# Kernel tuning notes

Hardware: AMD Instinct MI355X
Metric: run time of the kernel (lower is better)

Reference implementation:

```python
import jax, jax.numpy as jnp
import numpy as np

B, S, E, H = 2, 2048, 1024, 16
D = E // H  # head_dim = 64
SCALE = 1.0 / np.sqrt(D)


def setup_inputs() -> dict:
    key = jax.random.key(0)
    ks = jax.random.split(key, 5)
    std = 0.02
    return {
        "x": jax.random.normal(ks[0], (B, S, E), dtype=jnp.float32),
        "wq": jax.random.normal(ks[1], (E, E), dtype=jnp.float32) * std,
        "wk": jax.random.normal(ks[2], (E, E), dtype=jnp.float32) * std,
        "wv": jax.random.normal(ks[3], (E, E), dtype=jnp.float32) * std,
        "wo": jax.random.normal(ks[4], (E, E), dtype=jnp.float32) * std,
    }


def reference(x, wq, wk, wv, wo):
    # Linear projections (torch Linear: y = x @ W.T); weights stored as [out, in]
    q = jnp.einsum('bse,fe->bsf', x, wq)
    k = jnp.einsum('bse,fe->bsf', x, wk)
    v = jnp.einsum('bse,fe->bsf', x, wv)
    # split heads -> [B, H, S, D]
    q = q.reshape(B, S, H, D).transpose(0, 2, 1, 3)
    k = k.reshape(B, S, H, D).transpose(0, 2, 1, 3)
    v = v.reshape(B, S, H, D).transpose(0, 2, 1, 3)
    # scaled dot-product scores [B, H, S, S]
    scores = jnp.einsum('bhqd,bhkd->bhqk', q, k) * SCALE
    # causal mask: -inf above diagonal
    causal = jnp.triu(jnp.full((S, S), -jnp.inf, dtype=scores.dtype), k=1)
    scores = scores + causal[None, None, :, :]
    attn = jax.nn.softmax(scores, axis=-1)
    # dropout p=0 -> identity
    out = jnp.einsum('bhqk,bhkd->bhqd', attn, v)
    out = out.transpose(0, 2, 1, 3).reshape(B, S, E)
    return jnp.einsum('bse,fe->bsf', out, wo)
```

## Files before the change

kernel.cpp:

```cpp
#include <hip/hip_runtime.h>
#include <hip/hip_bf16.h>

#define B_ 2
#define S_ 2048
#define E_ 1024
#define H_ 16
#define D_ 64
#define QKV_N 3072
#define C2_ 0.18033688011112042f

typedef __attribute__((ext_vector_type(8))) unsigned short ushort8_t;
typedef __attribute__((ext_vector_type(8))) short short8_t;
typedef __attribute__((ext_vector_type(4))) float f32x4;

__device__ __forceinline__ unsigned short f2b(float f) {
    union { float f; unsigned u; } x; x.f = f;
    unsigned r = x.u + 0x7FFFu + ((x.u >> 16) & 1u);
    return (unsigned short)(r >> 16);
}
__device__ __forceinline__ ushort2 pkbf(float a, float b) {
    union { __hip_bfloat162 h; ushort2 u; } c;
    c.h = __float22bfloat162_rn(make_float2(a, b));
    return c.u;
}
__device__ __forceinline__ void glds16(const unsigned short* g, unsigned short* l) {
    __builtin_amdgcn_global_load_lds((const __attribute__((address_space(1))) void*)g,
                                     (__attribute__((address_space(3))) void*)l, 16, 0, 0);
}

__global__ __launch_bounds__(256) void cast_all(const float* __restrict__ x,
                                                const float* __restrict__ wq,
                                                const float* __restrict__ wk,
                                                const float* __restrict__ wv,
                                                const float* __restrict__ wo,
                                                unsigned short* __restrict__ xb,
                                                unsigned short* __restrict__ wb) {
    int idx = blockIdx.x * 256 + threadIdx.x;
    const float* src; unsigned short* dst; float s = 1.f; int j;
    if (idx < 1048576) {
        src = x; dst = xb; j = idx;
    } else {
        j = idx - 1048576;
        int y = j >> 18;
        src = (y == 0) ? wq : (y == 1) ? wk : (y == 2) ? wv : wo;
        dst = wb + (size_t)y * 1048576;
        j &= 262143;
        if (y == 0) s = C2_;
    }
    float4 v = ((const float4*)src)[j];
    ushort2 lo = pkbf(v.x * s, v.y * s), hi = pkbf(v.z * s, v.w * s);
    ((ushort4*)dst)[j] = make_ushort4(lo.x, lo.y, hi.x, hi.y);
}

template <int TM, bool OUT_BF16, bool VT>
__device__ __forceinline__ void gemm_bt_body(const unsigned short* __restrict__ A,
                                             const unsigned short* __restrict__ Bt,
                                             void* __restrict__ Cout,
                                             int m0, int n0, int N, int K) {
    __shared__ unsigned short As[2 * TM * 32];
    __shared__ unsigned short Bs[2 * 128 * 32];
    const int tid = threadIdx.x;
    const int wave = tid >> 6;
    const int lane = tid & 63;
    const int wm = (wave >> 1) * (TM / 2);
    const int wn = (wave & 1) * 64;
    const int quad = lane >> 4;
    const int l15 = lane & 15;
    constexpr int MI = TM / 32;

    f32x4 acc[MI][4] = {};

    const int srow = lane >> 2;
    const int scb  = (lane & 3) * 8;
    const unsigned short* gB0 = Bt + (size_t)(n0 + wave * 32 + srow) * K + scb;
    const unsigned short* gB1 = gB0 + (size_t)16 * K;
    unsigned short* lB0 = Bs + wave * 1024;
    unsigned short* lB1 = lB0 + 512;
    const unsigned short* gA0;
    const unsigned short* gA1 = nullptr;
    unsigned short* lA0;
    unsigned short* lA1 = nullptr;
    if (TM == 128) {
        gA0 = A + (size_t)(m0 + wave * 32 + srow) * K + scb;
        gA1 = gA0 + (size_t)16 * K;
        lA0 = As + wave * 1024; lA1 = lA0 + 512;
    } else {
        gA0 = A + (size_t)(m0 + wave * 16 + srow) * K + scb;
        lA0 = As + wave * 512;
    }

    for (int k0 = 0; k0 < K; k0 += 64) {
        __syncthreads();
        glds16(gA0 + k0, lA0);
        glds16(gA0 + k0 + 32, lA0 + TM * 32);
        if (TM == 128) {
            glds16(gA1 + k0, lA1);
            glds16(gA1 + k0 + 32, lA1 + TM * 32);
        }
        glds16(gB0 + k0, lB0);
        glds16(gB0 + k0 + 32, lB0 + 128 * 32);
        glds16(gB1 + k0, lB1);
        glds16(gB1 + k0 + 32, lB1 + 128 * 32);
        __syncthreads();

#pragma unroll
        for (int h = 0; h < 2; ++h) {
            const unsigned short* ah = As + h * TM * 32;
            const unsigned short* bh = Bs + h * 128 * 32;
            short8_t af[MI], bfv[4];
#pragma unroll
            for (int mi = 0; mi < MI; ++mi)
                af[mi] = *(const short8_t*)(&ah[(wm + mi * 16 + l15) * 32 + quad * 8]);
#pragma unroll
            for (int ni = 0; ni < 4; ++ni)
                bfv[ni] = *(const short8_t*)(&bh[(wn + ni * 16 + l15) * 32 + quad * 8]);
#pragma unroll
            for (int mi = 0; mi < MI; ++mi)
#pragma unroll
                for (int ni = 0; ni < 4; ++ni)
                    acc[mi][ni] = __builtin_amdgcn_mfma_f32_16x16x32_bf16(
                        af[mi], bfv[ni], acc[mi][ni], 0, 0, 0);
        }
    }

    if (VT && n0 >= 2048) {
#pragma unroll
        for (int mi = 0; mi < MI; ++mi)
#pragma unroll
            for (int ni = 0; ni < 4; ++ni) {
                int col = n0 + wn + ni * 16 + l15;
                int r0  = m0 + wm + mi * 16 + quad * 4;
                int bb  = r0 >> 11, s = r0 & 2047;
                size_t drow = (size_t)bb * 2048 + 2 * (col - 2048) + (s >> 10);
                unsigned short* dp = (unsigned short*)Cout + drow * QKV_N + 2048 + (s & 1023);
                *(ushort4*)dp = make_ushort4(f2b(acc[mi][ni][0]), f2b(acc[mi][ni][1]),
                                             f2b(acc[mi][ni][2]), f2b(acc[mi][ni][3]));
            }
        return;
    }

#pragma unroll
    for (int mi = 0; mi < MI; ++mi)
#pragma unroll
        for (int ni = 0; ni < 4; ++ni)
#pragma unroll
            for (int r = 0; r < 4; ++r) {
                int row = m0 + wm + mi * 16 + quad * 4 + r;
                int col = n0 + wn + ni * 16 + l15;
                float val = acc[mi][ni][r];
                if (OUT_BF16)
                    ((unsigned short*)Cout)[(size_t)row * N + col] = f2b(val);
                else
                    ((float*)Cout)[(size_t)row * N + col] = val;
            }
}

__global__ __launch_bounds__(256, 3) void gemm_qkv(const unsigned short* __restrict__ xb,
                                                   const unsigned short* __restrict__ wqkv,
                                                   unsigned short* __restrict__ qkv) {
    int id = blockIdx.x + 24 * blockIdx.y;
    int sw = (id & 7) * 96 + (id >> 3);
    int n0 = (sw % 24) * 128;
    int m0 = (sw / 24) * 128;
    gemm_bt_body<128, true, true>(xb, wqkv, qkv, m0, n0, QKV_N, E_);
}

__global__ __launch_bounds__(256, 2) void gemm_out(const unsigned short* __restrict__ a,
                                                   const unsigned short* __restrict__ wob,
                                                   float* __restrict__ c) {
    gemm_bt_body<64, false, false>(a, wob, c, blockIdx.y * 64, blockIdx.x * 128, E_, E_);
}

__global__ __launch_bounds__(512, 4) void attn_kernel(const unsigned short* __restrict__ QKV,
                                                      unsigned short* __restrict__ O) {
    __shared__ unsigned short Ks[2][64 * 64];
    __shared__ unsigned short Vs[2][64 * 64];
    __shared__ unsigned short Ps[8][16 * 64];

    const int b = blockIdx.z, h = blockIdx.y;
    const int cx = blockIdx.x;
    const int c0 = (cx & 1) ? (15 - (cx >> 1)) : (cx >> 1);
    const int c = (b == 0) ? c0 : (15 - c0);
    const int tid = threadIdx.x;
    const int w = tid >> 6, lane = tid & 63;
    const int quad = lane >> 4, l15 = lane & 15;
    const int lx = l15 & 7;
    const int chunk = (w < 4) ? (31 - c) : c;
    const int Q0 = chunk * 64 + (w & 3) * 16;

    const size_t qo = (size_t)(b * S_ + Q0 + l15) * QKV_N + h * D_;
    short8_t bq0 = *(const short8_t*)(QKV + qo + quad * 8);
    short8_t bq1 = *(const short8_t*)(QKV + qo + 32 + quad * 8);

    f32x4 Oacc[4] = {};
    f32x4 Lacc = {};
    const int qg = Q0 + l15;
    short8_t ones;
#pragma unroll
    for (int i = 0; i < 8; ++i) ones[i] = (short)0x3F80;

    const int fo0 = ((quad) ^ lx) * 8;
    const int fo1 = ((4 + quad) ^ lx) * 8;
    const int krow = l15 * 64;
    int pwo[4];
#pragma unroll
    for (int tm = 0; tm < 4; ++tm)
        pwo[tm] = ((tm * 2 + (quad >> 1)) ^ lx) * 8 + (quad & 1) * 4;

    const int srow = tid >> 3;
    const int scb  = tid & 7;
    const int scw  = (scb ^ (srow & 7)) * 8;
    const int wofs = w * 512;
    const unsigned short* KsrcB = QKV + (size_t)(b * S_ + srow) * QKV_N + 1024 + h * D_ + scw;
    const unsigned short* VsrcB = QKV + (size_t)(b * S_ + 2 * (h * D_ + srow)) * QKV_N + 2048 + scw;

    auto issue = [&](int pn, int ktn) {
        glds16(KsrcB + (size_t)ktn * QKV_N, &Ks[pn][wofs]);
        glds16(VsrcB + (size_t)(ktn >> 10) * QKV_N + (ktn & 1023), &Vs[pn][wofs]);
    };

    const int ntiles = 32 - c;
    issue(0, 0);

    for (int t = 0; t < ntiles; ++t) {
        const int p = t & 1;
        const int kt = t * 64;
        __syncthreads();
        if (t + 1 < ntiles) issue(p ^ 1, kt + 64);
        __builtin_amdgcn_sched_barrier(0);

        if (kt > Q0 + 15) continue;
        const bool h2 = (kt + 32 <= Q0 + 15);

        if (kt + 63 <= Q0) {
#pragma unroll
            for (int tm = 0; tm < 4; ++tm) {
                short8_t ak0 = *(const short8_t*)(&Ks[p][tm * 1024 + krow + fo0]);
                short8_t ak1 = *(const short8_t*)(&Ks[p][tm * 1024 + krow + fo1]);
                f32x4 st = {0.f, 0.f, 0.f, 0.f};
                __builtin_amdgcn_s_setprio(1);
                st = __builtin_amdgcn_mfma_f32_16x16x32_bf16(ak0, bq0, st, 0, 0, 0);
                st = __builtin_amdgcn_mfma_f32_16x16x32_bf16(ak1, bq1, st, 0, 0, 0);
                __builtin_amdgcn_s_setprio(0);
                float p0 = __builtin_amdgcn_exp2f(st[0]);
                float p1 = __builtin_amdgcn_exp2f(st[1]);
                float p2 = __builtin_amdgcn_exp2f(st[2]);
                float p3 = __builtin_amdgcn_exp2f(st[3]);
                ushort2 a = pkbf(p0, p1), c2 = pkbf(p2, p3);
                *(ushort4*)(&Ps[w][krow + pwo[tm]]) = make_ushort4(a.x, a.y, c2.x, c2.y);
            }
        } else {
            const int need = h2 ? 4 : 2;
            for (int tm = 0; tm < need; ++tm) {
                if (kt + tm * 16 <= Q0 + 15) {
                    short8_t ak0 = *(const short8_t*)(&Ks[p][tm * 1024 + krow + fo0]);
                    short8_t ak1 = *(const short8_t*)(&Ks[p][tm * 1024 + krow + fo1]);
                    f32x4 st = {0.f, 0.f, 0.f, 0.f};
                    __builtin_amdgcn_s_setprio(1);
                    st = __builtin_amdgcn_mfma_f32_16x16x32_bf16(ak0, bq0, st, 0, 0, 0);
                    st = __builtin_amdgcn_mfma_f32_16x16x32_bf16(ak1, bq1, st, 0, 0, 0);
                    __builtin_amdgcn_s_setprio(0);
                    const int kvb = kt + tm * 16 + quad * 4;
                    float p0 = (kvb     > qg) ? 0.f : __builtin_amdgcn_exp2f(st[0]);
                    float p1 = (kvb + 1 > qg) ? 0.f : __builtin_amdgcn_exp2f(st[1]);
                    float p2 = (kvb + 2 > qg) ? 0.f : __builtin_amdgcn_exp2f(st[2]);
                    float p3 = (kvb + 3 > qg) ? 0.f : __builtin_amdgcn_exp2f(st[3]);
                    ushort2 a = pkbf(p0, p1), c2 = pkbf(p2, p3);
                    *(ushort4*)(&Ps[w][krow + pwo[tm]]) = make_ushort4(a.x, a.y, c2.x, c2.y);
                } else {
                    *(ushort4*)(&Ps[w][krow + pwo[tm]]) = make_ushort4(0, 0, 0, 0);
                }
            }
        }

#pragma unroll
        for (int kh = 0; kh < 2; ++kh) {
            if (kh == 1 && !h2) break;
            const int fo = kh ? fo1 : fo0;
            short8_t bv[4];
#pragma unroll
            for (int tn = 0; tn < 4; ++tn)
                bv[tn] = *(const short8_t*)(&Vs[p][tn * 1024 + krow + fo]);
            short8_t ap = *(const short8_t*)(&Ps[w][krow + fo]);
            __builtin_amdgcn_s_setprio(1);
#pragma unroll
            for (int tn = 0; tn < 4; ++tn)
                Oacc[tn] = __builtin_amdgcn_mfma_f32_16x16x32_bf16(
                    ap, bv[tn], Oacc[tn], 0, 0, 0);
            Lacc = __builtin_amdgcn_mfma_f32_16x16x32_bf16(ap, ones, Lacc, 0, 0, 0);
            __builtin_amdgcn_s_setprio(0);
        }
    }

    float lir[4];
#pragma unroll
    for (int r = 0; r < 4; ++r)
        lir[r] = 1.f / Lacc[r];
#pragma unroll
    for (int tn = 0; tn < 4; ++tn)
#pragma unroll
        for (int r = 0; r < 4; ++r) {
            int row = Q0 + quad * 4 + r;
            O[(size_t)(b * S_ + row) * E_ + h * D_ + tn * 16 + l15] =
                f2b(Oacc[tn][r] * lir[r]);
        }
}

extern "C" void kernel_launch(void* const* d_in, const int* in_sizes, int n_in,
                              void* d_out, int out_size, void* d_ws, size_t ws_size,
                              hipStream_t stream) {
    const float* x  = (const float*)d_in[0];
    const float* wq = (const float*)d_in[1];
    const float* wk = (const float*)d_in[2];
    const float* wv = (const float*)d_in[3];
    const float* wo = (const float*)d_in[4];
    float* out = (float*)d_out;

    unsigned short* ws   = (unsigned short*)d_ws;
    unsigned short* xb   = ws;
    unsigned short* wqkv = ws + 4194304;
    unsigned short* wob  = ws + 7340032;
    unsigned short* qkvb = ws + 8388608;
    unsigned short* ab   = ws + 20971520;

    cast_all<<<8192, 256, 0, stream>>>(x, wq, wk, wv, wo, xb, wqkv);
    gemm_qkv<<<dim3(24, 32), 256, 0, stream>>>(xb, wqkv, qkvb);
    attn_kernel<<<dim3(16, 16, 2), 512, 0, stream>>>(qkvb, ab);
    gemm_out<<<dim3(8, 64), 256, 0, stream>>>(ab, wob, out);
}
```

Measured before the change: 171.2 us.

## Triple-buffer K/V tiles in attention with vmcnt waits; swizzle out-projection block order

The attention kernel moves from double to triple buffering of K/V tiles in shared memory, prefetching two tiles ahead. The full __syncthreads is replaced by an explicit s_waitcnt vmcnt plus s_barrier, so loads for later tiles can stay in flight while the current tile is computed. The out-projection GEMM also gets a block-index swizzle to improve L2 reuse. The extra LDS buffers raise shared memory per block, which may cut occupancy. The hand-written vmcnt counts must match the number of outstanding global-to-LDS loads for correctness.

Result: faster. 167.0 us (-2.4%).

```diff
diff --git a/kernel.cpp b/kernel.cpp
--- a/kernel.cpp
+++ b/kernel.cpp
@@ -168,13 +168,15 @@
 __global__ __launch_bounds__(256, 2) void gemm_out(const unsigned short* __restrict__ a,
                                                    const unsigned short* __restrict__ wob,
                                                    float* __restrict__ c) {
-    gemm_bt_body<64, false, false>(a, wob, c, blockIdx.y * 64, blockIdx.x * 128, E_, E_);
+    int id = blockIdx.x + 8 * blockIdx.y;
+    int sw = (id & 7) * 64 + (id >> 3);
+    gemm_bt_body<64, false, false>(a, wob, c, (sw >> 3) * 64, (sw & 7) * 128, E_, E_);
 }
 
 __global__ __launch_bounds__(512, 4) void attn_kernel(const unsigned short* __restrict__ QKV,
                                                       unsigned short* __restrict__ O) {
-    __shared__ unsigned short Ks[2][64 * 64];
-    __shared__ unsigned short Vs[2][64 * 64];
+    __shared__ unsigned short Ks[3][64 * 64];
+    __shared__ unsigned short Vs[3][64 * 64];
     __shared__ unsigned short Ps[8][16 * 64];
 
     const int b = blockIdx.z, h = blockIdx.y;
@@ -214,82 +216,91 @@
     const unsigned short* KsrcB = QKV + (size_t)(b * S_ + srow) * QKV_N + 1024 + h * D_ + scw;
     const unsigned short* VsrcB = QKV + (size_t)(b * S_ + 2 * (h * D_ + srow)) * QKV_N + 2048 + scw;
 
-    auto issue = [&](int pn, int ktn) {
-        glds16(KsrcB + (size_t)ktn * QKV_N, &Ks[pn][wofs]);
-        glds16(VsrcB + (size_t)(ktn >> 10) * QKV_N + (ktn & 1023), &Vs[pn][wofs]);
+    auto issue = [&](int bn, int ktn) {
+        glds16(KsrcB + (size_t)ktn * QKV_N, &Ks[bn][wofs]);
+        glds16(VsrcB + (size_t)(ktn >> 10) * QKV_N + (ktn & 1023), &Vs[bn][wofs]);
     };
 
     const int ntiles = 32 - c;
     issue(0, 0);
+    issue(1, 64);
+    int bi = 0;
 
     for (int t = 0; t < ntiles; ++t) {
-        const int p = t & 1;
         const int kt = t * 64;
-        __syncthreads();
-        if (t + 1 < ntiles) issue(p ^ 1, kt + 64);
+        if (t + 1 < ntiles) asm volatile("s_waitcnt vmcnt(2)" ::: "memory");
+        else                asm volatile("s_waitcnt vmcnt(0)" ::: "memory");
+        __builtin_amdgcn_s_barrier();
         __builtin_amdgcn_sched_barrier(0);
-
-        if (kt > Q0 + 15) continue;
-        const bool h2 = (kt + 32 <= Q0 + 15);
-
-        if (kt + 63 <= Q0) {
-#pragma unroll
-            for (int tm = 0; tm < 4; ++tm) {
-                short8_t ak0 = *(const short8_t*)(&Ks[p][tm * 1024 + krow + fo0]);
-                short8_t ak1 = *(const short8_t*)(&Ks[p][tm * 1024 + krow + fo1]);
-                f32x4 st = {0.f, 0.f, 0.f, 0.f};
-                __builtin_amdgcn_s_setprio(1);
-                st = __builtin_amdgcn_mfma_f32_16x16x32_bf16(ak0, bq0, st, 0, 0, 0);
-                st = __builtin_amdgcn_mfma_f32_16x16x32_bf16(ak1, bq1, st, 0, 0, 0);
-                __builtin_amdgcn_s_setprio(0);
-                float p0 = __builtin_amdgcn_exp2f(st[0]);
-                float p1 = __builtin_amdgcn_exp2f(st[1]);
-                float p2 = __builtin_amdgcn_exp2f(st[2]);
-                float p3 = __builtin_amdgcn_exp2f(st[3]);
-                ushort2 a = pkbf(p0, p1), c2 = pkbf(p2, p3);
-                *(ushort4*)(&Ps[w][krow + pwo[tm]]) = make_ushort4(a.x, a.y, c2.x, c2.y);
-            }
-        } else {
-            const int need = h2 ? 4 : 2;
-            for (int tm = 0; tm < need; ++tm) {
-                if (kt + tm * 16 <= Q0 + 15) {
-                    short8_t ak0 = *(const short8_t*)(&Ks[p][tm * 1024 + krow + fo0]);
-                    short8_t ak1 = *(const short8_t*)(&Ks[p][tm * 1024 + krow + fo1]);
+        if (t + 2 < ntiles) {
+            int b2 = bi + 2; if (b2 >= 3) b2 -= 3;
+            issue(b2, kt + 128);
+        }
+
+        if (kt <= Q0 + 15) {
+            const bool h2 = (kt + 32 <= Q0 + 15);
+
+            if (kt + 63 <= Q0) {
+#pragma unroll
+                for (int tm = 0; tm < 4; ++tm) {
+                    short8_t ak0 = *(const short8_t*)(&Ks[bi][tm * 1024 + krow + fo0]);
+                    short8_t ak1 = *(const short8_t*)(&Ks[bi][tm * 1024 + krow + fo1]);
                     f32x4 st = {0.f, 0.f, 0.f, 0.f};
                     __builtin_amdgcn_s_setprio(1);
                     st = __builtin_amdgcn_mfma_f32_16x16x32_bf16(ak0, bq0, st, 0, 0, 0);
                     st = __builtin_amdgcn_mfma_f32_16x16x32_bf16(ak1, bq1, st, 0, 0, 0);
                     __builtin_amdgcn_s_setprio(0);
-                    const int kvb = kt + tm * 16 + quad * 4;
-                    float p0 = (kvb     > qg) ? 0.f : __builtin_amdgcn_exp2f(st[0]);
-                    float p1 = (kvb + 1 > qg) ? 0.f : __builtin_amdgcn_exp2f(st[1]);
-                    float p2 = (kvb + 2 > qg) ? 0.f : __builtin_amdgcn_exp2f(st[2]);
-                    float p3 = (kvb + 3 > qg) ? 0.f : __builtin_amdgcn_exp2f(st[3]);
+                    float p0 = __builtin_amdgcn_exp2f(st[0]);
+                    float p1 = __builtin_amdgcn_exp2f(st[1]);
+                    float p2 = __builtin_amdgcn_exp2f(st[2]);
+                    float p3 = __builtin_amdgcn_exp2f(st[3]);
                     ushort2 a = pkbf(p0, p1), c2 = pkbf(p2, p3);
                     *(ushort4*)(&Ps[w][krow + pwo[tm]]) = make_ushort4(a.x, a.y, c2.x, c2.y);
-                } else {
-                    *(ushort4*)(&Ps[w][krow + pwo[tm]]) = make_ushort4(0, 0, 0, 0);
+                }
+            } else {
+                const int need = h2 ? 4 : 2;
+                for (int tm = 0; tm < need; ++tm) {
+                    if (kt + tm * 16 <= Q0 + 15) {
+                        short8_t ak0 = *(const short8_t*)(&Ks[bi][tm * 1024 + krow + fo0]);
+                        short8_t ak1 = *(const short8_t*)(&Ks[bi][tm * 1024 + krow + fo1]);
+                        f32x4 st = {0.f, 0.f, 0.f, 0.f};
+                        __builtin_amdgcn_s_setprio(1);
+                        st = __builtin_amdgcn_mfma_f32_16x16x32_bf16(ak0, bq0, st, 0, 0, 0);
+                        st = __builtin_amdgcn_mfma_f32_16x16x32_bf16(ak1, bq1, st, 0, 0, 0);
+                        __builtin_amdgcn_s_setprio(0);
+                        const int kvb = kt + tm * 16 + quad * 4;
+                        float p0 = (kvb     > qg) ? 0.f : __builtin_amdgcn_exp2f(st[0]);
+                        float p1 = (kvb + 1 > qg) ? 0.f : __builtin_amdgcn_exp2f(st[1]);
+                        float p2 = (kvb + 2 > qg) ? 0.f : __builtin_amdgcn_exp2f(st[2]);
+                        float p3 = (kvb + 3 > qg) ? 0.f : __builtin_amdgcn_exp2f(st[3]);
+                        ushort2 a = pkbf(p0, p1), c2 = pkbf(p2, p3);
+                        *(ushort4*)(&Ps[w][krow + pwo[tm]]) = make_ushort4(a.x, a.y, c2.x, c2.y);
+                    } else {
+                        *(ushort4*)(&Ps[w][krow + pwo[tm]]) = make_ushort4(0, 0, 0, 0);
+                    }
                 }
             }
-        }
-
-#pragma unroll
-        for (int kh = 0; kh < 2; ++kh) {
-            if (kh == 1 && !h2) break;
-            const int fo = kh ? fo1 : fo0;
-            short8_t bv[4];
-#pragma unroll
-            for (int tn = 0; tn < 4; ++tn)
-                bv[tn] = *(const short8_t*)(&Vs[p][tn * 1024 + krow + fo]);
-            short8_t ap = *(const short8_t*)(&Ps[w][krow + fo]);
-            __builtin_amdgcn_s_setprio(1);
-#pragma unroll
-            for (int tn = 0; tn < 4; ++tn)
-                Oacc[tn] = __builtin_amdgcn_mfma_f32_16x16x32_bf16(
-                    ap, bv[tn], Oacc[tn], 0, 0, 0);
-            Lacc = __builtin_amdgcn_mfma_f32_16x16x32_bf16(ap, ones, Lacc, 0, 0, 0);
-            __builtin_amdgcn_s_setprio(0);
-        }
+
+#pragma unroll
+            for (int kh = 0; kh < 2; ++kh) {
+                if (kh == 1 && !h2) break;
+                const int fo = kh ? fo1 : fo0;
+                short8_t bv[4];
+#pragma unroll
+                for (int tn = 0; tn < 4; ++tn)
+                    bv[tn] = *(const short8_t*)(&Vs[bi][tn * 1024 + krow + fo]);
+                short8_t ap = *(const short8_t*)(&Ps[w][krow + fo]);
+                __builtin_amdgcn_s_setprio(1);
+#pragma unroll
+                for (int tn = 0; tn < 4; ++tn)
+                    Oacc[tn] = __builtin_amdgcn_mfma_f32_16x16x32_bf16(
+                        ap, bv[tn], Oacc[tn], 0, 0, 0);
+                Lacc = __builtin_amdgcn_mfma_f32_16x16x32_bf16(ap, ones, Lacc, 0, 0, 0);
+                __builtin_amdgcn_s_setprio(0);
+            }
+        }
+
+        bi = (bi + 1 == 3) ? 0 : bi + 1;
     }
 
     float lir[4];
```
